# Optimization experiments

Hardware: AMD Instinct MI355X
Metric: run time of the kernel (lower is better)

The kernel has to match this reference:

```python
import jax, jax.numpy as jnp
import numpy as np

HIDDEN = 4096
N_HEADS = 32
N_KV_HEADS = 8
HEAD_DIM = HIDDEN // N_HEADS
ROPE_BASE = 10000.0


def rotate_half(x):
    x1, x2 = jnp.split(x, 2, axis=-1)
    return jnp.concatenate((-x2, x1), axis=-1)


def rope_cos_sin(seq_len, dtype=jnp.float32):
    inv_freq = 1.0 / (ROPE_BASE ** (jnp.arange(0, HEAD_DIM, 2, dtype=jnp.float32) / HEAD_DIM))
    t = jnp.arange(seq_len, dtype=jnp.float32)
    freqs = jnp.einsum('i,j->ij', t, inv_freq)          # [S, D/2]
    emb = jnp.concatenate((freqs, freqs), axis=-1)       # [S, D]
    return jnp.cos(emb).astype(dtype), jnp.sin(emb).astype(dtype)


def setup_inputs() -> dict:
    key = jax.random.key(0)
    ks = jax.random.split(key, 6)
    bsz, q_len = 2, 2048
    hidden_states = jax.random.normal(ks[0], (bsz, q_len, HIDDEN), dtype=jnp.float32)
    # causal additive mask [bsz, 1, q, kv]
    neg = jnp.finfo(jnp.float32).min
    causal = jnp.where(jnp.tril(jnp.ones((q_len, q_len), dtype=bool)), 0.0, neg)
    attention_mask = jnp.broadcast_to(causal, (bsz, 1, q_len, q_len)).astype(jnp.float32)
    position_ids = jnp.broadcast_to(jnp.arange(q_len, dtype=jnp.int64), (bsz, q_len))
    s = 1.0 / np.sqrt(HIDDEN)
    Wq = jax.random.normal(ks[1], (HIDDEN, N_HEADS * HEAD_DIM), dtype=jnp.float32) * s
    Wk = jax.random.normal(ks[2], (HIDDEN, N_KV_HEADS * HEAD_DIM), dtype=jnp.float32) * s
    Wv = jax.random.normal(ks[3], (HIDDEN, N_KV_HEADS * HEAD_DIM), dtype=jnp.float32) * s
    Wo = jax.random.normal(ks[4], (N_HEADS * HEAD_DIM, HIDDEN), dtype=jnp.float32) * s
    return {"hidden_states": hidden_states, "attention_mask": attention_mask,
            "position_ids": position_ids, "Wq": Wq, "Wk": Wk, "Wv": Wv, "Wo": Wo}


def reference(hidden_states, attention_mask, position_ids, Wq, Wk, Wv, Wo):
    bsz, q_len, _ = hidden_states.shape
    groups = N_HEADS // N_KV_HEADS
    q = (hidden_states @ Wq).reshape(bsz, q_len, N_HEADS, HEAD_DIM).transpose(0, 2, 1, 3)
    k = (hidden_states @ Wk).reshape(bsz, q_len, N_KV_HEADS, HEAD_DIM).transpose(0, 2, 1, 3)
    v = (hidden_states @ Wv).reshape(bsz, q_len, N_KV_HEADS, HEAD_DIM).transpose(0, 2, 1, 3)
    cos, sin = rope_cos_sin(q_len, hidden_states.dtype)
    cos = cos[position_ids][:, None]  # [B,1,S,D]
    sin = sin[position_ids][:, None]
    q = q * cos + rotate_half(q) * sin
    k = k * cos + rotate_half(k) * sin
    # GQA: repeat_interleave KV heads
    k = jnp.repeat(k, groups, axis=1)
    v = jnp.repeat(v, groups, axis=1)
    scores = jnp.einsum('bhqd,bhkd->bhqk', q, k) / np.sqrt(HEAD_DIM)
    scores = scores + attention_mask
    attn = jax.nn.softmax(scores.astype(jnp.float32), axis=-1).astype(q.dtype)
    out = jnp.einsum('bhqk,bhkd->bhqd', attn, v)
    out = out.transpose(0, 2, 1, 3).reshape(bsz, q_len, HIDDEN)
    return out @ Wo
```

## Files before the change

kernel.cpp:

```cpp
#include <hip/hip_runtime.h>
#include <cstdint>
#include <type_traits>

typedef unsigned short u16;
typedef __attribute__((ext_vector_type(8))) short bf16x8;
typedef __attribute__((ext_vector_type(4))) float f32x4;

__device__ __forceinline__ u16 f2bf(float f) {
  unsigned u = __float_as_uint(f);
  u += 0x7fffu + ((u >> 16) & 1u);
  return (u16)(u >> 16);
}
__device__ __forceinline__ float bf2f(u16 h) {
  return __uint_as_float(((unsigned)h) << 16);
}
__device__ __forceinline__ unsigned cvtpk(float lo, float hi) {
  unsigned r;
  asm("v_cvt_pk_bf16_f32 %0, %1, %2" : "=v"(r) : "v"(lo), "v"(hi));
  return r;
}

__device__ __forceinline__ void glds16(const u16* g, u16* l) {
  __builtin_amdgcn_global_load_lds((const __attribute__((address_space(1))) void*)g,
                                   (__attribute__((address_space(3))) void*)l,
                                   16, 0, 0);
}

__global__ __launch_bounds__(256) void k_f32_to_bf16(const float* __restrict__ in,
                                                     u16* __restrict__ out, int n4) {
  int i = blockIdx.x * 256 + threadIdx.x;
  if (i < n4) {
    float4 v = ((const float4*)in)[i];
    ushort4 o;
    o.x = f2bf(v.x); o.y = f2bf(v.y); o.z = f2bf(v.z); o.w = f2bf(v.w);
    ((ushort4*)out)[i] = o;
  }
}

__global__ __launch_bounds__(256) void k_transpose_f32_bf16(const float* __restrict__ in,
                                                            u16* __restrict__ out,
                                                            int R, int C) {
  __shared__ float t[32][33];
  int tx = threadIdx.x & 31, ty = threadIdx.x >> 5;
  int c0 = blockIdx.x * 32, r0 = blockIdx.y * 32;
#pragma unroll
  for (int i = 0; i < 4; ++i)
    t[ty + 8 * i][tx] = in[(size_t)(r0 + ty + 8 * i) * C + c0 + tx];
  __syncthreads();
#pragma unroll
  for (int i = 0; i < 4; ++i)
    out[(size_t)(c0 + ty + 8 * i) * R + r0 + tx] = f2bf(t[tx][ty + 8 * i]);
}

template <typename OutT>
__global__ __launch_bounds__(256) void k_gemm_bt(const u16* __restrict__ A,
                                                 const u16* __restrict__ B,
                                                 OutT* __restrict__ C,
                                                 int M, int N, int K) {
  __shared__ __align__(16) u16 As[128][32];
  __shared__ __align__(16) u16 Bs[128][32];
  int tid = threadIdx.x;
  int wave = tid >> 6, lane = tid & 63, quad = lane >> 4, l15 = lane & 15;
  int m0 = blockIdx.y * 128, n0 = blockIdx.x * 128;
  int wm = (wave >> 1) * 64, wn = (wave & 1) * 64;

  int rowoff = lane >> 2;
  int gcol = (((lane & 3) ^ ((lane >> 3) & 3)) * 8);
  const u16* Ag = A + (size_t)(m0 + wave * 32 + rowoff) * K + gcol;
  const u16* Bg = B + (size_t)(n0 + wave * 32 + rowoff) * K + gcol;
  u16* AsBase = &As[wave * 32][0];
  u16* BsBase = &Bs[wave * 32][0];
  const size_t rstride = (size_t)16 * K;

  int rchunk = (quad ^ ((l15 >> 1) & 3)) * 8;

  f32x4 acc[4][4] = {};
  for (int k0 = 0; k0 < K; k0 += 32) {
    __syncthreads();
    glds16(Ag + k0, AsBase);
    glds16(Ag + k0 + rstride, AsBase + 16 * 32);
    glds16(Bg + k0, BsBase);
    glds16(Bg + k0 + rstride, BsBase + 16 * 32);
    __syncthreads();
    bf16x8 af[4], bfr[4];
#pragma unroll
    for (int i = 0; i < 4; ++i) {
      af[i]  = *(const bf16x8*)&As[wm + i * 16 + l15][rchunk];
      bfr[i] = *(const bf16x8*)&Bs[wn + i * 16 + l15][rchunk];
    }
#pragma unroll
    for (int mt = 0; mt < 4; ++mt)
#pragma unroll
      for (int nt = 0; nt < 4; ++nt)
        acc[mt][nt] = __builtin_amdgcn_mfma_f32_16x16x32_bf16(af[mt], bfr[nt], acc[mt][nt], 0, 0, 0);
  }
#pragma unroll
  for (int mt = 0; mt < 4; ++mt)
#pragma unroll
    for (int nt = 0; nt < 4; ++nt) {
      int row = m0 + wm + mt * 16 + quad * 4;
      int col = n0 + wn + nt * 16 + l15;
#pragma unroll
      for (int r = 0; r < 4; ++r) {
        float v = acc[mt][nt][r];
        if constexpr (std::is_same<OutT, u16>::value)
          C[(size_t)(row + r) * N + col] = f2bf(v);
        else
          C[(size_t)(row + r) * N + col] = v;
      }
    }
}

__global__ __launch_bounds__(256) void k_rope(u16* __restrict__ qkv) {
  int row = blockIdx.x;
  int s = row & 2047;
  u16* base = qkv + (size_t)row * 6144;
  for (int p = threadIdx.x; p < 2560; p += 256) {
    int d, col;
    if (p < 2048) { d = p & 63; col = (p >> 6) * 128 + d; }
    else { int pk = p - 2048; d = pk & 63; col = 4096 + (pk >> 6) * 128 + d; }
    float f = exp2f((float)d * (-13.287712379549449f / 64.0f));
    float th = (float)s * f;
    float c = cosf(th), sn = sinf(th);
    float x1 = bf2f(base[col]), x2 = bf2f(base[col + 64]);
    base[col]      = f2bf(x1 * c - x2 * sn);
    base[col + 64] = f2bf(x2 * c + x1 * sn);
  }
}

__global__ __launch_bounds__(256) void k_vt(const u16* __restrict__ qkv, u16* __restrict__ vt) {
  __shared__ u16 t[32][33];
  int tx = threadIdx.x & 31, ty = threadIdx.x >> 5;
  int s0 = blockIdx.x * 32, d0 = blockIdx.y * 32, g = blockIdx.z;
  int b = g >> 3, kvh = g & 7;
  const u16* in = qkv + (size_t)(b * 2048) * 6144 + 5120 + kvh * 128;
  u16* out = vt + (size_t)g * 128 * 2048;
#pragma unroll
  for (int i = 0; i < 4; ++i)
    t[ty + 8 * i][tx] = in[(size_t)(s0 + ty + 8 * i) * 6144 + d0 + tx];
  __syncthreads();
#pragma unroll
  for (int i = 0; i < 4; ++i)
    out[(size_t)(d0 + ty + 8 * i) * 2048 + s0 + tx] = t[tx][ty + 8 * i];
}

__global__ __launch_bounds__(256) void k_flash(const u16* __restrict__ qkv,
                                               const u16* __restrict__ vt,
                                               u16* __restrict__ ao) {
  __shared__ __align__(16) u16 Ks[64][128];
  __shared__ __align__(16) u16 Vs[128][64];
  __shared__ __align__(16) u16 Ps[4][16][64];
  const int tid = threadIdx.x, wave = tid >> 6, lane = tid & 63;
  const int quad = lane >> 4, l15 = lane & 15, l7 = l15 & 7;
  const int bh = blockIdx.x, b = bh >> 5, h = bh & 31, kvh = h >> 2;
  const int q0 = (31 - (int)blockIdx.y) * 64;

  bf16x8 aq[4];
  {
    const u16* qp = qkv + (size_t)(b * 2048 + q0 + wave * 16 + l15) * 6144 + h * 128 + quad * 8;
#pragma unroll
    for (int c = 0; c < 4; ++c) aq[c] = *(const bf16x8*)(qp + c * 32);
  }

  f32x4 oacc[8] = {};
  float m_r = -1e30f, l_r = 0.f;

  const u16* kbase = qkv + (size_t)(b * 2048) * 6144 + 4096 + kvh * 128;
  const u16* vbase = vt + (size_t)(b * 8 + kvh) * 128 * 2048;

  const int krow = wave * 4 + (lane >> 4);
  const int kch = (lane & 15) ^ (krow & 7);
  const u16* ksrc0 = kbase + (size_t)krow * 6144 + kch * 8;
  const int vrow = wave * 8 + (lane >> 3);
  const int vch = (lane & 7) ^ (vrow & 7);
  const u16* vsrc0 = vbase + (size_t)vrow * 2048 + vch * 8;
  u16* KsW = &Ks[0][0] + wave * 512;
  u16* VsW = &Vs[0][0] + wave * 512;

  const float SC = 0.12751744f;
  const int qg = q0 + wave * 16 + l15;
  const int nk = q0 / 64 + 1;

  for (int kt = 0; kt < nk; ++kt) {
    const int k0 = kt * 64;
    __syncthreads();
#pragma unroll
    for (int it = 0; it < 4; ++it)
      glds16(ksrc0 + (size_t)(k0 + it * 16) * 6144, KsW + it * 2048);
#pragma unroll
    for (int it = 0; it < 4; ++it)
      glds16(vsrc0 + k0 + it * 65536, VsW + it * 2048);
    __syncthreads();

    f32x4 sacc[4] = {};
    __builtin_amdgcn_s_setprio(1);
#pragma unroll
    for (int c = 0; c < 4; ++c)
#pragma unroll
      for (int nt = 0; nt < 4; ++nt) {
        const bf16x8 bk = *(const bf16x8*)&Ks[nt * 16 + l15][((4 * c + quad) ^ l7) * 8];
        sacc[nt] = __builtin_amdgcn_mfma_f32_16x16x32_bf16(bk, aq[c], sacc[nt], 0, 0, 0);
      }
    __builtin_amdgcn_s_setprio(0);

    float p[16];
    if (kt == nk - 1) {
#pragma unroll
      for (int nt = 0; nt < 4; ++nt)
#pragma unroll
        for (int r = 0; r < 4; ++r) {
          const float v = sacc[nt][r] * SC;
          p[nt * 4 + r] = (k0 + nt * 16 + quad * 4 + r > qg) ? -3e38f : v;
        }
    } else {
#pragma unroll
      for (int nt = 0; nt < 4; ++nt)
#pragma unroll
        for (int r = 0; r < 4; ++r) p[nt * 4 + r] = sacc[nt][r] * SC;
    }

    float rm = p[0];
#pragma unroll
    for (int i = 1; i < 16; ++i) rm = fmaxf(rm, p[i]);
    rm = fmaxf(rm, __shfl_xor(rm, 16, 64));
    rm = fmaxf(rm, __shfl_xor(rm, 32, 64));

    if (__any(rm > m_r + 8.0f)) {
      const float mn = fmaxf(m_r, rm);
      const float alpha = exp2f(m_r - mn);
      m_r = mn;
      l_r *= alpha;
#pragma unroll
      for (int r = 0; r < 4; ++r) {
        const float ar = __shfl(alpha, quad * 4 + r, 64);
#pragma unroll
        for (int o = 0; o < 8; ++o) oacc[o][r] *= ar;
      }
    }

    float rs = 0.f;
#pragma unroll
    for (int i = 0; i < 16; ++i) { p[i] = exp2f(p[i] - m_r); rs += p[i]; }
    rs += __shfl_xor(rs, 16, 64);
    rs += __shfl_xor(rs, 32, 64);
    l_r += rs;

    char* psrow = (char*)&Ps[wave][0][0] + l15 * 128;
#pragma unroll
    for (int nt = 0; nt < 4; ++nt)
#pragma unroll
      for (int pr = 0; pr < 2; ++pr) {
        const unsigned pk = cvtpk(p[nt * 4 + pr * 2], p[nt * 4 + pr * 2 + 1]);
        const int csw = (2 * nt + (quad >> 1)) ^ l7;
        *(unsigned*)(psrow + csw * 16 + (quad & 1) * 8 + pr * 4) = pk;
      }

    __builtin_amdgcn_s_setprio(1);
#pragma unroll
    for (int kc = 0; kc < 2; ++kc) {
      const int cs = (4 * kc + quad) ^ l7;
      const bf16x8 ap = *(const bf16x8*)(psrow + cs * 16);
#pragma unroll
      for (int o = 0; o < 8; ++o) {
        const bf16x8 bv = *(const bf16x8*)&Vs[o * 16 + l15][cs * 8];
        oacc[o] = __builtin_amdgcn_mfma_f32_16x16x32_bf16(ap, bv, oacc[o], 0, 0, 0);
      }
    }
    __builtin_amdgcn_s_setprio(0);
  }

  const float inv = 1.0f / l_r;
  u16* op = ao + (size_t)(b * 2048 + q0 + wave * 16 + quad * 4) * 4096 + h * 128 + l15;
#pragma unroll
  for (int r = 0; r < 4; ++r) {
    const float ir = __shfl(inv, quad * 4 + r, 64);
#pragma unroll
    for (int o = 0; o < 8; ++o)
      op[(size_t)r * 4096 + o * 16] = f2bf(oacc[o][r] * ir);
  }
}

extern "C" void kernel_launch(void* const* d_in, const int* in_sizes, int n_in,
                              void* d_out, int out_size, void* d_ws, size_t ws_size,
                              hipStream_t stream) {
  const float* X  = (const float*)d_in[0];
  const float* Wq = (const float*)d_in[3];
  const float* Wk = (const float*)d_in[4];
  const float* Wv = (const float*)d_in[5];
  const float* Wo = (const float*)d_in[6];
  float* out = (float*)d_out;

  char* ws = (char*)d_ws;
  u16* Xb     = (u16*)(ws);
  u16* WqkvT  = (u16*)(ws + 33554432ull);
  u16* WoT    = (u16*)(ws + 83886080ull);
  u16* QKV    = (u16*)(ws + 117440512ull);
  u16* Vt     = (u16*)(ws + 167772160ull);
  u16* AO     = (u16*)(ws + 176160768ull);

  k_f32_to_bf16<<<16384, 256, 0, stream>>>(X, Xb, 4194304);
  k_transpose_f32_bf16<<<dim3(128, 128), 256, 0, stream>>>(Wq, WqkvT, 4096, 4096);
  k_transpose_f32_bf16<<<dim3(32, 128), 256, 0, stream>>>(Wk, WqkvT + (size_t)4096 * 4096, 4096, 1024);
  k_transpose_f32_bf16<<<dim3(32, 128), 256, 0, stream>>>(Wv, WqkvT + (size_t)5120 * 4096, 4096, 1024);
  k_transpose_f32_bf16<<<dim3(128, 128), 256, 0, stream>>>(Wo, WoT, 4096, 4096);
  k_gemm_bt<u16><<<dim3(48, 32), 256, 0, stream>>>(Xb, WqkvT, QKV, 4096, 6144, 4096);
  k_rope<<<4096, 256, 0, stream>>>(QKV);
  k_vt<<<dim3(64, 4, 16), 256, 0, stream>>>(QKV, Vt);
  k_flash<<<dim3(64, 32), 256, 0, stream>>>(QKV, Vt, AO);
  k_gemm_bt<float><<<dim3(32, 32), 256, 0, stream>>>(AO, WoT, out, 4096, 4096, 4096);
}
```

Baseline: 855.0 us.

## Replace GEMM with 256x256 double-buffered pipelined kernel using 8 waves

Swaps the simple 128x128 single-buffered bf16 GEMM for a 256x256 tile kernel with 512 threads, BK=64, and double-buffered LDS. Global-to-LDS loads for the next tile are interleaved with the MFMA phases, and vmcnt waits plus barriers replace full syncthreads. A grouped block-index swizzle is added for L2 locality. This aims to hide memory latency and raise arithmetic intensity. In exchange it uses 128KB of LDS and more registers per block, and the grid becomes small (256 or 384 blocks), which can underfill the CUs.

```diff
diff --git a/kernel.cpp b/kernel.cpp
--- a/kernel.cpp
+++ b/kernel.cpp
@@ -25,6 +25,8 @@
                                    (__attribute__((address_space(3))) void*)l,
                                    16, 0, 0);
 }
+
+#define MFMA16(a, b, c) __builtin_amdgcn_mfma_f32_16x16x32_bf16((a), (b), (c), 0, 0, 0)
 
 __global__ __launch_bounds__(256) void k_f32_to_bf16(const float* __restrict__ in,
                                                      u16* __restrict__ out, int n4) {
@@ -53,56 +55,125 @@
 }
 
 template <typename OutT>
-__global__ __launch_bounds__(256) void k_gemm_bt(const u16* __restrict__ A,
-                                                 const u16* __restrict__ B,
-                                                 OutT* __restrict__ C,
-                                                 int M, int N, int K) {
-  __shared__ __align__(16) u16 As[128][32];
-  __shared__ __align__(16) u16 Bs[128][32];
-  int tid = threadIdx.x;
-  int wave = tid >> 6, lane = tid & 63, quad = lane >> 4, l15 = lane & 15;
-  int m0 = blockIdx.y * 128, n0 = blockIdx.x * 128;
-  int wm = (wave >> 1) * 64, wn = (wave & 1) * 64;
-
-  int rowoff = lane >> 2;
-  int gcol = (((lane & 3) ^ ((lane >> 3) & 3)) * 8);
-  const u16* Ag = A + (size_t)(m0 + wave * 32 + rowoff) * K + gcol;
-  const u16* Bg = B + (size_t)(n0 + wave * 32 + rowoff) * K + gcol;
-  u16* AsBase = &As[wave * 32][0];
-  u16* BsBase = &Bs[wave * 32][0];
-  const size_t rstride = (size_t)16 * K;
-
-  int rchunk = (quad ^ ((l15 >> 1) & 3)) * 8;
-
-  f32x4 acc[4][4] = {};
-  for (int k0 = 0; k0 < K; k0 += 32) {
-    __syncthreads();
-    glds16(Ag + k0, AsBase);
-    glds16(Ag + k0 + rstride, AsBase + 16 * 32);
-    glds16(Bg + k0, BsBase);
-    glds16(Bg + k0 + rstride, BsBase + 16 * 32);
-    __syncthreads();
-    bf16x8 af[4], bfr[4];
-#pragma unroll
-    for (int i = 0; i < 4; ++i) {
-      af[i]  = *(const bf16x8*)&As[wm + i * 16 + l15][rchunk];
-      bfr[i] = *(const bf16x8*)&Bs[wn + i * 16 + l15][rchunk];
-    }
-#pragma unroll
-    for (int mt = 0; mt < 4; ++mt)
-#pragma unroll
-      for (int nt = 0; nt < 4; ++nt)
-        acc[mt][nt] = __builtin_amdgcn_mfma_f32_16x16x32_bf16(af[mt], bfr[nt], acc[mt][nt], 0, 0, 0);
-  }
-#pragma unroll
-  for (int mt = 0; mt < 4; ++mt)
-#pragma unroll
-    for (int nt = 0; nt < 4; ++nt) {
-      int row = m0 + wm + mt * 16 + quad * 4;
-      int col = n0 + wn + nt * 16 + l15;
+__global__ __launch_bounds__(512, 2) void k_gemm256(const u16* __restrict__ A,
+                                                    const u16* __restrict__ B,
+                                                    OutT* __restrict__ C,
+                                                    int M, int N, int K) {
+  __shared__ __align__(16) u16 lds[65536];
+  const int tid = threadIdx.x, wave = tid >> 6, lane = tid & 63;
+  const int quad = lane >> 4, l15 = lane & 15, l7 = l15 & 7;
+  const int wr = wave >> 2, wc = wave & 3;
+
+  const int nwg = gridDim.x * gridDim.y;
+  const int bid = blockIdx.y * gridDim.x + blockIdx.x;
+  const int swz = (bid & 7) * (nwg >> 3) + (bid >> 3);
+  const int m0 = (swz / gridDim.x) * 256, n0 = (swz % gridDim.x) * 256;
+
+  const int lrow = lane >> 3, lx = (lane & 7) ^ lrow;
+  const size_t rowK = (size_t)K;
+  const u16* Abase = A + (size_t)(m0 + wr * 128 + (wave & 3) * 8 + lrow) * rowK + lx * 8;
+  const u16* Bbase = B + (size_t)(n0 + wave * 16 + lrow) * rowK + lx * 8;
+
+  u16* const AT0 = lds;
+  u16* const BT0 = lds + 16384;
+  u16* const AT1 = lds + 32768;
+  u16* const BT1 = lds + 49152;
+  const int adst = (wr * 128 + (wave & 3) * 8) * 64;
+  const int bdst = wave * 16 * 64;
+
+#define STAGE_A(DST, la, kk) \
+  glds16(Abase + (size_t)((la) * 32) * rowK + (kk), (DST) + adst + (la) * 2048)
+#define STAGE_B(DST, g, kk)                                                      \
+  glds16(Bbase + (size_t)((((g) >> 1) * 128 + ((g) & 1) * 8)) * rowK + (kk),     \
+         (DST) + bdst + (((g) >> 1) * 128 + ((g) & 1) * 8) * 64)
+
+  const int aoff = (wr * 128 + l15) * 64;
+  const int boff = (wc * 64 + l15) * 64;
+  const int ck0 = (quad ^ l7) * 8;
+  const int ck1 = ((quad + 4) ^ l7) * 8;
+
+  STAGE_B(BT0, 0, 0); STAGE_B(BT0, 1, 0); STAGE_B(BT0, 2, 0); STAGE_B(BT0, 3, 0);
+  STAGE_A(AT0, 0, 0); STAGE_A(AT0, 1, 0); STAGE_A(AT0, 2, 0); STAGE_A(AT0, 3, 0);
+  f32x4 acc[8][4] = {};
+  asm volatile("s_waitcnt vmcnt(3)\ns_barrier" ::: "memory");
+
+#define GPHASE(MP, STG1, STG2, VN)                                              \
+  {                                                                             \
+    bf16x8 a00 = *(const bf16x8*)&AT[aoff + (2 * (MP)) * 1024 + ck0];           \
+    bf16x8 a01 = *(const bf16x8*)&AT[aoff + (2 * (MP)) * 1024 + ck1];           \
+    bf16x8 a10 = *(const bf16x8*)&AT[aoff + (2 * (MP) + 1) * 1024 + ck0];       \
+    bf16x8 a11 = *(const bf16x8*)&AT[aoff + (2 * (MP) + 1) * 1024 + ck1];       \
+    STG1;                                                                       \
+    STG2;                                                                       \
+    asm volatile("s_barrier" ::: "memory");                                     \
+    asm volatile("s_waitcnt lgkmcnt(0)" ::: "memory");                          \
+    __builtin_amdgcn_sched_barrier(0);                                          \
+    __builtin_amdgcn_s_setprio(1);                                              \
+    _Pragma("unroll")                                                           \
+    for (int nf = 0; nf < 4; ++nf) {                                            \
+      acc[2 * (MP)][nf] = MFMA16(a00, bq[nf][0], acc[2 * (MP)][nf]);            \
+      acc[2 * (MP)][nf] = MFMA16(a01, bq[nf][1], acc[2 * (MP)][nf]);            \
+      acc[2 * (MP) + 1][nf] = MFMA16(a10, bq[nf][0], acc[2 * (MP) + 1][nf]);    \
+      acc[2 * (MP) + 1][nf] = MFMA16(a11, bq[nf][1], acc[2 * (MP) + 1][nf]);    \
+    }                                                                           \
+    __builtin_amdgcn_s_setprio(0);                                              \
+    asm volatile("s_waitcnt vmcnt(" #VN ")\ns_barrier" ::: "memory");           \
+  }
+
+  const int nt = K >> 6;
+  for (int kt = 0; kt < nt; ++kt) {
+    u16* const AT = (kt & 1) ? AT1 : AT0;
+    u16* const BT = (kt & 1) ? BT1 : BT0;
+    u16* const ATn = (kt & 1) ? AT0 : AT1;
+    u16* const BTn = (kt & 1) ? BT0 : BT1;
+    const int kk = (kt + 1 < nt) ? ((kt + 1) << 6) : 0;
+
+    bf16x8 bq[4][2];
+    {
+      bf16x8 a00 = *(const bf16x8*)&AT[aoff + 0 * 1024 + ck0];
+      bf16x8 a01 = *(const bf16x8*)&AT[aoff + 0 * 1024 + ck1];
+      bf16x8 a10 = *(const bf16x8*)&AT[aoff + 1 * 1024 + ck0];
+      bf16x8 a11 = *(const bf16x8*)&AT[aoff + 1 * 1024 + ck1];
+#pragma unroll
+      for (int nf = 0; nf < 4; ++nf) {
+        bq[nf][0] = *(const bf16x8*)&BT[boff + nf * 1024 + ck0];
+        bq[nf][1] = *(const bf16x8*)&BT[boff + nf * 1024 + ck1];
+      }
+      STAGE_B(BTn, 0, kk);
+      STAGE_B(BTn, 1, kk);
+      asm volatile("s_barrier" ::: "memory");
+      asm volatile("s_waitcnt lgkmcnt(0)" ::: "memory");
+      __builtin_amdgcn_sched_barrier(0);
+      __builtin_amdgcn_s_setprio(1);
+#pragma unroll
+      for (int nf = 0; nf < 4; ++nf) {
+        acc[0][nf] = MFMA16(a00, bq[nf][0], acc[0][nf]);
+        acc[0][nf] = MFMA16(a01, bq[nf][1], acc[0][nf]);
+        acc[1][nf] = MFMA16(a10, bq[nf][0], acc[1][nf]);
+        acc[1][nf] = MFMA16(a11, bq[nf][1], acc[1][nf]);
+      }
+      __builtin_amdgcn_s_setprio(0);
+      asm volatile("s_waitcnt vmcnt(4)\ns_barrier" ::: "memory");
+    }
+    GPHASE(1, STAGE_B(BTn, 2, kk), STAGE_B(BTn, 3, kk), 5)
+    GPHASE(2, STAGE_A(ATn, 0, kk), STAGE_A(ATn, 1, kk), 6)
+    GPHASE(3, STAGE_A(ATn, 2, kk), STAGE_A(ATn, 3, kk), 3)
+  }
+#undef GPHASE
+#undef STAGE_A
+#undef STAGE_B
+
+  asm volatile("s_waitcnt vmcnt(0)" ::: "memory");
+
+#pragma unroll
+  for (int mf = 0; mf < 8; ++mf)
+#pragma unroll
+    for (int nf = 0; nf < 4; ++nf) {
+      const int row = m0 + wr * 128 + mf * 16 + quad * 4;
+      const int col = n0 + wc * 64 + nf * 16 + l15;
 #pragma unroll
       for (int r = 0; r < 4; ++r) {
-        float v = acc[mt][nt][r];
+        float v = acc[mf][nf][r];
         if constexpr (std::is_same<OutT, u16>::value)
           C[(size_t)(row + r) * N + col] = f2bf(v);
         else
@@ -303,9 +374,9 @@
   k_transpose_f32_bf16<<<dim3(32, 128), 256, 0, stream>>>(Wk, WqkvT + (size_t)4096 * 4096, 4096, 1024);
   k_transpose_f32_bf16<<<dim3(32, 128), 256, 0, stream>>>(Wv, WqkvT + (size_t)5120 * 4096, 4096, 1024);
   k_transpose_f32_bf16<<<dim3(128, 128), 256, 0, stream>>>(Wo, WoT, 4096, 4096);
-  k_gemm_bt<u16><<<dim3(48, 32), 256, 0, stream>>>(Xb, WqkvT, QKV, 4096, 6144, 4096);
+  k_gemm256<u16><<<dim3(24, 16), 512, 0, stream>>>(Xb, WqkvT, QKV, 4096, 6144, 4096);
   k_rope<<<4096, 256, 0, stream>>>(QKV);
   k_vt<<<dim3(64, 4, 16), 256, 0, stream>>>(QKV, Vt);
   k_flash<<<dim3(64, 32), 256, 0, stream>>>(QKV, Vt, AO);
-  k_gemm_bt<float><<<dim3(32, 32), 256, 0, stream>>>(AO, WoT, out, 4096, 4096, 4096);
-}
+  k_gemm256<float><<<dim3(16, 16), 512, 0, stream>>>(AO, WoT, out, 4096, 4096, 4096);
+}
```

Result: faster. 748.1 us (-12.5%).
